# Kernel optimization log

Measured on AMD Instinct MI355X. Metric: run time of the kernel, lower is better.

Reference implementation:

```python
import jax, jax.numpy as jnp
import numpy as np

HEADS = 16
DIM_HEAD = 64
SEG = 512            # total_segment_len (num_longterm_mem_tokens = 0)
THETA = 10000.0
NEG_INF = -1e30


def _rotate_half(t):
    # interleaved pair rotation, as in rotary-embedding-torch
    t2 = t.reshape(*t.shape[:-1], t.shape[-1] // 2, 2)
    return jnp.stack((-t2[..., 1], t2[..., 0]), axis=-1).reshape(t.shape)


def setup_inputs() -> dict:
    key = jax.random.key(0)
    ks = jax.random.split(key, 4)
    b, n, d = 2, 4096, 1024
    dim_inner = HEADS * DIM_HEAD
    seq = jax.random.normal(ks[0], (b, n, d), dtype=jnp.float32)
    g_norm = jnp.ones((d,), dtype=jnp.float32)
    W_qkv = jax.random.normal(ks[1], (d, 3 * dim_inner), dtype=jnp.float32) * (d ** -0.5)
    W_out = jax.random.normal(ks[2], (dim_inner, d), dtype=jnp.float32) * (dim_inner ** -0.5)
    pm = jax.random.normal(ks[3], (2, HEADS, 16, DIM_HEAD), dtype=jnp.float32) * 0.02
    return {"seq": seq, "g_norm": g_norm, "W_qkv": W_qkv, "W_out": W_out, "pm": pm}


def reference(seq, g_norm, W_qkv, W_out, pm):
    b, n_tot, dim = seq.shape
    p = pm.shape[2]
    dh = DIM_HEAD

    # RMSNorm (elementwise affine, eps = dtype eps as in torch default)
    eps = jnp.asarray(jnp.finfo(seq.dtype).eps, seq.dtype)
    x = seq * jax.lax.rsqrt(jnp.mean(seq * seq, axis=-1, keepdims=True) + eps) * g_norm

    qkv = x @ W_qkv                                   # [b, n, 3*h*dh]
    q, k, v = jnp.split(qkv, 3, axis=-1)

    def split_heads(t):
        return t.reshape(b, n_tot, HEADS, dh).transpose(0, 2, 1, 3)  # b h n d

    q, k, v = map(split_heads, (q, k, v))

    # rotary over global positions (applied before segmenting)
    pos = jnp.arange(n_tot, dtype=seq.dtype)
    inv_freq = 1.0 / (THETA ** (jnp.arange(0, dh, 2, dtype=seq.dtype) / dh))
    ang = jnp.repeat(pos[:, None] * inv_freq, 2, axis=-1)            # [n, dh]
    cos, sin = jnp.cos(ang), jnp.sin(ang)
    q = q * cos + _rotate_half(q) * sin
    k = k * cos + _rotate_half(k) * sin

    # fold segments into batch: b h (w n) d -> (b w) h n d
    w = n_tot // SEG
    def seg_fold(t):
        return t.reshape(b, HEADS, w, SEG, dh).transpose(0, 2, 1, 3, 4).reshape(b * w, HEADS, SEG, dh)
    q, k, v = map(seg_fold, (q, k, v))

    # prepend persistent memory kv
    pmk = jnp.broadcast_to(pm[0], (b * w, HEADS, p, dh))
    pmv = jnp.broadcast_to(pm[1], (b * w, HEADS, p, dh))
    k = jnp.concatenate((pmk, k), axis=-2)            # [(bw), h, p+n, d]
    v = jnp.concatenate((pmv, v), axis=-2)

    scores = jnp.einsum('bhid,bhjd->bhij', q, k) * (dh ** -0.5)
    i = jnp.arange(SEG)[:, None]
    j = jnp.arange(SEG + p)[None, :]
    mask = (j < p) | ((j - p) <= i)                   # persistent mem always visible, causal in-segment
    scores = jnp.where(mask, scores, NEG_INF)
    attn = jax.nn.softmax(scores, axis=-1)
    out = jnp.einsum('bhij,bhjd->bhid', attn, v)      # [(bw), h, n, d]

    out = out.transpose(0, 2, 1, 3).reshape(b * w, SEG, HEADS * dh)
    out = out @ W_out
    return out.reshape(b, n_tot, dim)
```

## Files before the change

kernel.cpp:

```cpp
#include <hip/hip_runtime.h>
#include <hip/hip_bf16.h>

typedef __attribute__((ext_vector_type(8))) short short8v;
typedef __attribute__((ext_vector_type(4))) float f32x4;

#define B_ 2
#define NTOK 4096
#define DMODEL 1024
#define HEADS_ 16
#define DH 64
#define SEG_ 512
#define PMEM 16
#define ROWS 8192
#define QKVC 3072

__global__ __launch_bounds__(256) void rmsnorm_bf16(const float* __restrict__ seq,
                                                    const float* __restrict__ g,
                                                    __hip_bfloat16* __restrict__ x) {
    int row = blockIdx.x;
    const float4* in = (const float4*)(seq + (size_t)row * DMODEL);
    int tid = threadIdx.x;
    float4 v = in[tid];
    float ss = v.x*v.x + v.y*v.y + v.z*v.z + v.w*v.w;
    #pragma unroll
    for (int off = 32; off >= 1; off >>= 1) ss += __shfl_xor(ss, off, 64);
    __shared__ float red[4];
    if ((tid & 63) == 0) red[tid >> 6] = ss;
    __syncthreads();
    float tot = red[0] + red[1] + red[2] + red[3];
    float scale = rsqrtf(tot * (1.0f/(float)DMODEL) + 1.1920929e-7f);
    float4 gv = ((const float4*)g)[tid];
    union { ushort4 u; __hip_bfloat16 h[4]; } pk;
    pk.h[0] = __float2bfloat16(v.x*scale*gv.x);
    pk.h[1] = __float2bfloat16(v.y*scale*gv.y);
    pk.h[2] = __float2bfloat16(v.z*scale*gv.z);
    pk.h[3] = __float2bfloat16(v.w*scale*gv.w);
    ((ushort4*)(x + (size_t)row * DMODEL))[tid] = pk.u;
}

__global__ __launch_bounds__(256) void transpose_bf16(const float* __restrict__ W,
                                                      __hip_bfloat16* __restrict__ Wt,
                                                      int K, int N) {
    __shared__ float t[32][33];
    int n0 = blockIdx.x * 32, k0 = blockIdx.y * 32;
    int c = threadIdx.x & 31, r = threadIdx.x >> 5;
    #pragma unroll
    for (int rr = 0; rr < 32; rr += 8)
        t[rr + r][c] = W[(size_t)(k0 + rr + r)*N + n0 + c];
    __syncthreads();
    #pragma unroll
    for (int rr = 0; rr < 32; rr += 8)
        Wt[(size_t)(n0 + rr + r)*K + k0 + c] = __float2bfloat16(t[c][rr + r]);
}

__global__ __launch_bounds__(256) void prep_kernel(float* __restrict__ tab,
                                                   const float* __restrict__ pm,
                                                   __hip_bfloat16* __restrict__ pmb) {
    int idx = blockIdx.x*256 + threadIdx.x;
    if (idx < NTOK*32) {
        int n = idx >> 5, p = idx & 31;
        float inv = powf(10000.f, -(float)p * (1.f/32.f));
        float a = (float)n * inv;
        float sn, cs;
        sincosf(a, &sn, &cs);
        tab[(size_t)n*64 + 2*p]     = cs;
        tab[(size_t)n*64 + 2*p + 1] = sn;
    } else {
        int j = idx - NTOK*32;
        pmb[j] = __float2bfloat16(pm[j]);
    }
}

__device__ __forceinline__ void gldl(const __hip_bfloat16* g, char* l) {
    __builtin_amdgcn_global_load_lds((const __attribute__((address_space(1))) void*)g,
                                     (__attribute__((address_space(3))) void*)l, 16, 0, 0);
}
__device__ __forceinline__ void storeC(float* p, float v) { *p = v; }
__device__ __forceinline__ void storeC(__hip_bfloat16* p, float v) { *p = __float2bfloat16(v); }

template<typename OutT, bool ROPE>
__global__ __launch_bounds__(256, 2) void gemm_t(const __hip_bfloat16* __restrict__ A,
                                                 const __hip_bfloat16* __restrict__ Bt,
                                                 OutT* __restrict__ C,
                                                 const float* __restrict__ tab,
                                                 int M, int N, int K) {
    __shared__ __hip_bfloat16 As[8192];
    __shared__ __hip_bfloat16 Bs[8192];
    const int tid = threadIdx.x;
    const int wid = tid >> 6, lane = tid & 63;
    const int q8 = gridDim.x >> 3;
    const int swz = (blockIdx.x & 7) * q8 + (blockIdx.x >> 3);
    const int nbx = N >> 7;
    const int bm = (swz / nbx) * 128, bn = (swz % nbx) * 128;
    const int wm = (wid >> 1) * 64, wn = (wid & 1) * 64;
    const int fr = lane & 15, g = lane >> 4;

    const __hip_bfloat16* Abase = A  + (size_t)bm * K;
    const __hip_bfloat16* Bbase = Bt + (size_t)bn * K;

    f32x4 acc[4][4];
    #pragma unroll
    for (int i = 0; i < 4; ++i)
        #pragma unroll
        for (int j = 0; j < 4; ++j)
            acc[i][j] = (f32x4){0.f, 0.f, 0.f, 0.f};

    const int srow_in = lane >> 2;
    const int scol8  = (lane & 3) * 8;

    for (int k0 = 0; k0 < K; k0 += 64) {
        #pragma unroll
        for (int m = 0; m < 4; ++m) {
            int p = m & 1, rg = (wid << 1) + (m >> 1);
            gldl(Abase + (size_t)(rg*16 + srow_in)*K + k0 + p*32 + scol8,
                 (char*)(As + p*4096 + rg*512 + lane*8));
        }
        #pragma unroll
        for (int m = 0; m < 4; ++m) {
            int p = m & 1, rg = (wid << 1) + (m >> 1);
            gldl(Bbase + (size_t)(rg*16 + srow_in)*K + k0 + p*32 + scol8,
                 (char*)(Bs + p*4096 + rg*512 + lane*8));
        }
        __syncthreads();

        short8v a[4][2], b[4][2];
        #pragma unroll
        for (int mt = 0; mt < 4; ++mt)
            #pragma unroll
            for (int ks = 0; ks < 2; ++ks)
                a[mt][ks] = *(const short8v*)&As[ks*4096 + (wm + mt*16 + fr)*32 + g*8];
        #pragma unroll
        for (int nt = 0; nt < 4; ++nt)
            #pragma unroll
            for (int ks = 0; ks < 2; ++ks)
                b[nt][ks] = *(const short8v*)&Bs[ks*4096 + (wn + nt*16 + fr)*32 + g*8];
        #pragma unroll
        for (int mt = 0; mt < 4; ++mt)
            #pragma unroll
            for (int nt = 0; nt < 4; ++nt)
                #pragma unroll
                for (int ks = 0; ks < 2; ++ks)
                    acc[mt][nt] = __builtin_amdgcn_mfma_f32_16x16x32_bf16(a[mt][ks], b[nt][ks], acc[mt][nt], 0, 0, 0);
        __syncthreads();
    }

    const int rsub = (lane >> 4) << 2;
    if (ROPE && bn < 2048) {
        #pragma unroll
        for (int mt = 0; mt < 4; ++mt) {
            int rbase = bm + wm + mt*16 + rsub;
            #pragma unroll
            for (int nt = 0; nt < 4; ++nt) {
                int col = bn + wn + nt*16 + fr;
                int d = col & 63;
                int dc = d & ~1;
                #pragma unroll
                for (int r = 0; r < 4; ++r) {
                    float v = acc[mt][nt][r];
                    float pv = __shfl_xor(v, 1, 64);
                    int n = (rbase + r) & (NTOK - 1);
                    const float* tb = tab + (size_t)n*64;
                    float cs = tb[dc], sn = tb[dc+1];
                    float o = v*cs + ((d & 1) ? pv*sn : -pv*sn);
                    storeC(&C[(size_t)(rbase + r)*N + col], (float)o);
                }
            }
        }
    } else {
        #pragma unroll
        for (int mt = 0; mt < 4; ++mt) {
            int rbase = bm + wm + mt*16 + rsub;
            #pragma unroll
            for (int nt = 0; nt < 4; ++nt) {
                int col = bn + wn + nt*16 + fr;
                #pragma unroll
                for (int r = 0; r < 4; ++r)
                    storeC(&C[(size_t)(rbase + r)*N + col], acc[mt][nt][r]);
            }
        }
    }
}

__device__ __forceinline__ void stage_load(const __hip_bfloat16* __restrict__ qkv,
                                           const __hip_bfloat16* __restrict__ pmb,
                                           int h, int srow, int tt, int skey, int sdg,
                                           uint4 kv[2]) {
    int kg = tt*64 + skey;
    if (kg < PMEM) {
        kv[0] = *(const uint4*)(pmb + ((size_t)h*PMEM + kg)*DH + sdg);
        kv[1] = *(const uint4*)(pmb + ((size_t)(HEADS_ + h)*PMEM + kg)*DH + sdg);
    } else {
        int r = min(kg - PMEM, SEG_ - 1);
        const __hip_bfloat16* bp = qkv + (size_t)(srow + r)*QKVC + h*DH + sdg;
        kv[0] = *(const uint4*)(bp + 1024);
        kv[1] = *(const uint4*)(bp + 2048);
    }
}

__device__ __forceinline__ void stage_write(char* Kb, char* Vb,
                                            int skey, int sdg, const uint4 kv[2]) {
    *(uint4*)(Kb + ((skey*128 + sdg*2) ^ ((skey&7)<<4))) = kv[0];
    union { uint4 u; ushort s[8]; } vv; vv.u = kv[1];
    #pragma unroll
    for (int j = 0; j < 8; ++j) {
        int d = sdg + j;
        *(ushort*)(Vb + ((d*128 + skey*2) ^ ((d&7)<<4))) = vv.s[j];
    }
}

__global__ __launch_bounds__(512, 2) void attn_mfma(const __hip_bfloat16* __restrict__ qkv,
                                                    const __hip_bfloat16* __restrict__ pmb,
                                                    __hip_bfloat16* __restrict__ ao) {
    __shared__ __hip_bfloat16 KB[2][4096];
    __shared__ __hip_bfloat16 VB[2][4096];
    __shared__ __hip_bfloat16 PB[8][1024];

    const int s = blockIdx.x, h = blockIdx.y, rb = blockIdx.z;
    const int srow = (s >> 3)*NTOK + (s & 7)*SEG_;
    const int tid = threadIdx.x;
    const int w = tid >> 6, lane = tid & 63;
    const int g = lane >> 4, fr = lane & 15;
    const int rsub = g * 4;
    char* Pw = (char*)&PB[w][0];

    const int grp0 = 2*w + rb;
    const int grp1 = 30 - 2*w + rb;
    const int tmax = 7 + rb;

    short8v aq[2][2];
    #pragma unroll
    for (int mt = 0; mt < 2; ++mt) {
        int grp = mt ? grp1 : grp0;
        const __hip_bfloat16* qp = qkv + (size_t)(srow + grp*16 + fr)*QKVC + h*DH;
        #pragma unroll
        for (int ks = 0; ks < 2; ++ks)
            aq[mt][ks] = *(const short8v*)(qp + ks*32 + g*8);
    }

    f32x4 accO[2][4];
    float m_[2][4], l_[2][4];
    #pragma unroll
    for (int mt = 0; mt < 2; ++mt) {
        #pragma unroll
        for (int dt = 0; dt < 4; ++dt) accO[mt][dt] = (f32x4){0.f,0.f,0.f,0.f};
        #pragma unroll
        for (int r = 0; r < 4; ++r) { m_[mt][r] = -1e30f; l_[mt][r] = 0.f; }
    }

    const int skey = tid >> 3, sdg = (tid & 7) * 8;

    {
        uint4 kv[2];
        stage_load(qkv, pmb, h, srow, 0, skey, sdg, kv);
        stage_write((char*)&KB[0][0], (char*)&VB[0][0], skey, sdg, kv);
    }
    __syncthreads();

    for (int t = 0; t <= tmax; ++t) {
        const int bf = t & 1;
        uint4 kvn[2];
        if (t < tmax) stage_load(qkv, pmb, h, srow, t + 1, skey, sdg, kvn);

        char* Kb = (char*)&KB[bf][0];
        char* Vb = (char*)&VB[bf][0];

        short8v bk[4][2];
        #pragma unroll
        for (int nt = 0; nt < 4; ++nt)
            #pragma unroll
            for (int ks = 0; ks < 2; ++ks) {
                int row = nt*16 + fr;
                bk[nt][ks] = *(const short8v*)(Kb + ((row*128 + ks*64 + g*16) ^ ((row&7)<<4)));
            }

        #pragma unroll
        for (int mt = 0; mt < 2; ++mt) {
            const int qb = (mt ? grp1 : grp0) * 16;
            if (t > 0 && t*64 > qb + 31) continue;

            f32x4 sA[4];
            #pragma unroll
            for (int nt = 0; nt < 4; ++nt) sA[nt] = (f32x4){0.f,0.f,0.f,0.f};
            __builtin_amdgcn_s_setprio(1);
            #pragma unroll
            for (int ks = 0; ks < 2; ++ks)
                #pragma unroll
                for (int nt = 0; nt < 4; ++nt)
                    sA[nt] = __builtin_amdgcn_mfma_f32_16x16x32_bf16(aq[mt][ks], bk[nt][ks], sA[nt], 0, 0, 0);
            __builtin_amdgcn_s_setprio(0);

            if (!(t*64 + 63 <= qb + 16)) {
                #pragma unroll
                for (int nt = 0; nt < 4; ++nt) {
                    int kg2 = t*64 + nt*16 + fr;
                    #pragma unroll
                    for (int r = 0; r < 4; ++r) {
                        int irow = qb + rsub + r;
                        if (!((kg2 < PMEM) || (kg2 <= irow + PMEM))) sA[nt][r] = -1e30f;
                    }
                }
            }

            float mx[4], corr[4];
            #pragma unroll
            for (int r = 0; r < 4; ++r)
                mx[r] = fmaxf(fmaxf(sA[0][r], sA[1][r]), fmaxf(sA[2][r], sA[3][r]));
            #pragma unroll
            for (int r = 0; r < 4; ++r) {
                #pragma unroll
                for (int off = 1; off <= 8; off <<= 1)
                    mx[r] = fmaxf(mx[r], __shfl_xor(mx[r], off, 64));
                float mn = fmaxf(m_[mt][r], mx[r]);
                corr[r] = __expf((m_[mt][r] - mn)*0.125f);
                m_[mt][r] = mn;
            }
            #pragma unroll
            for (int nt = 0; nt < 4; ++nt)
                #pragma unroll
                for (int r = 0; r < 4; ++r)
                    sA[nt][r] = __expf((sA[nt][r] - m_[mt][r])*0.125f);
            #pragma unroll
            for (int r = 0; r < 4; ++r) {
                float lp = sA[0][r] + sA[1][r] + sA[2][r] + sA[3][r];
                l_[mt][r] = l_[mt][r]*corr[r] + lp;
            }
            #pragma unroll
            for (int dt = 0; dt < 4; ++dt)
                #pragma unroll
                for (int r = 0; r < 4; ++r)
                    accO[mt][dt][r] *= corr[r];

            #pragma unroll
            for (int nt = 0; nt < 4; ++nt)
                #pragma unroll
                for (int r = 0; r < 4; ++r) {
                    int row_l = rsub + r;
                    *(__hip_bfloat16*)(Pw + ((row_l*128 + (nt*16 + fr)*2) ^ ((row_l&7)<<4))) =
                        __float2bfloat16(sA[nt][r]);
                }

            __builtin_amdgcn_s_setprio(1);
            #pragma unroll
            for (int ks2 = 0; ks2 < 2; ++ks2) {
                short8v ap = *(const short8v*)(Pw + ((fr*128 + ks2*64 + g*16) ^ ((fr&7)<<4)));
                #pragma unroll
                for (int dt = 0; dt < 4; ++dt) {
                    int vrow = dt*16 + fr;
                    short8v bv = *(const short8v*)(Vb + ((vrow*128 + ks2*64 + g*16) ^ ((vrow&7)<<4)));
                    accO[mt][dt] = __builtin_amdgcn_mfma_f32_16x16x32_bf16(ap, bv, accO[mt][dt], 0, 0, 0);
                }
            }
            __builtin_amdgcn_s_setprio(0);
        }

        if (t < tmax) stage_write((char*)&KB[bf^1][0], (char*)&VB[bf^1][0], skey, sdg, kvn);
        __syncthreads();
    }

    #pragma unroll
    for (int mt = 0; mt < 2; ++mt) {
        const int grp = mt ? grp1 : grp0;
        float inv[4];
        #pragma unroll
        for (int r = 0; r < 4; ++r) {
            float lt = l_[mt][r];
            #pragma unroll
            for (int off = 1; off <= 8; off <<= 1) lt += __shfl_xor(lt, off, 64);
            inv[r] = 1.0f / lt;
        }
        #pragma unroll
        for (int dt = 0; dt < 4; ++dt)
            #pragma unroll
            for (int r = 0; r < 4; ++r) {
                int row_l = rsub + r;
                *(__hip_bfloat16*)(Pw + ((row_l*128 + (dt*16 + fr)*2) ^ ((row_l&7)<<4))) =
                    __float2bfloat16(accO[mt][dt][r] * inv[r]);
            }
        #pragma unroll
        for (int c = 0; c < 2; ++c) {
            int row_l = c*8 + (lane >> 3);
            size_t grow = (size_t)(srow + grp*16 + row_l);
            uint4 v = *(const uint4*)(Pw + ((row_l*128 + (lane&7)*16) ^ ((row_l&7)<<4)));
            *(uint4*)((char*)(ao + grow*DMODEL + h*DH) + (lane&7)*16) = v;
        }
    }
}

extern "C" void kernel_launch(void* const* d_in, const int* in_sizes, int n_in,
                              void* d_out, int out_size, void* d_ws, size_t ws_size,
                              hipStream_t stream) {
    const float* seq  = (const float*)d_in[0];
    const float* g    = (const float*)d_in[1];
    const float* wqkv = (const float*)d_in[2];
    const float* wout = (const float*)d_in[3];
    const float* pm   = (const float*)d_in[4];
    float* out = (float*)d_out;

    char* ws = (char*)d_ws;
    __hip_bfloat16* qkvb  = (__hip_bfloat16*)ws;
    __hip_bfloat16* xb    = (__hip_bfloat16*)(ws + 50331648);
    __hip_bfloat16* wqkvt = (__hip_bfloat16*)(ws + 50331648 + 16777216);
    __hip_bfloat16* woutt = (__hip_bfloat16*)(ws + 50331648 + 16777216 + 6291456);
    float* tab            = (float*)(ws + 50331648 + 16777216 + 6291456 + 2097152);
    __hip_bfloat16* pmb   = (__hip_bfloat16*)(ws + 50331648 + 16777216 + 6291456 + 2097152 + 1048576);

    prep_kernel<<<(NTOK*32 + 2*HEADS_*PMEM*DH)/256, 256, 0, stream>>>(tab, pm, pmb);
    transpose_bf16<<<dim3(QKVC/32, DMODEL/32), 256, 0, stream>>>(wqkv, wqkvt, DMODEL, QKVC);
    transpose_bf16<<<dim3(DMODEL/32, DMODEL/32), 256, 0, stream>>>(wout, woutt, DMODEL, DMODEL);
    rmsnorm_bf16<<<ROWS, 256, 0, stream>>>(seq, g, xb);
    gemm_t<__hip_bfloat16, true><<<(QKVC/128)*(ROWS/128), 256, 0, stream>>>(xb, wqkvt, qkvb, tab, ROWS, QKVC, DMODEL);
    attn_mfma<<<dim3(16, 16, 2), 512, 0, stream>>>(qkvb, pmb, xb);
    gemm_t<float, false><<<(DMODEL/128)*(ROWS/128), 256, 0, stream>>>(xb, woutt, out, nullptr, ROWS, DMODEL, DMODEL);
}
```

Measured before the change: 175.2 us.

## Swizzle GEMM LDS layout and stage QKV epilogue through LDS for vector stores

Merges the A and B shared buffers into one byte array and loads each 128x64 tile as full 128-byte rows with an XOR swizzle on the 16-byte column chunk, so the MFMA fragment reads avoid LDS bank conflicts. For the RoPE/QKV GEMM, the epilogue now writes bf16 results into swizzled shared memory and then copies them out with coalesced 16-byte global stores instead of scattered 2-byte stores. It also reads the cos/sin pair as one float2. The epilogue adds an extra barrier and assumes the output type is bf16 whenever ROPE is set.

```diff
diff --git a/kernel.cpp b/kernel.cpp
--- a/kernel.cpp
+++ b/kernel.cpp
@@ -84,8 +84,7 @@
                                                  OutT* __restrict__ C,
                                                  const float* __restrict__ tab,
                                                  int M, int N, int K) {
-    __shared__ __hip_bfloat16 As[8192];
-    __shared__ __hip_bfloat16 Bs[8192];
+    __shared__ __align__(16) char smem[32768];
     const int tid = threadIdx.x;
     const int wid = tid >> 6, lane = tid & 63;
     const int q8 = gridDim.x >> 3;
@@ -95,8 +94,10 @@
     const int wm = (wid >> 1) * 64, wn = (wid & 1) * 64;
     const int fr = lane & 15, g = lane >> 4;
 
-    const __hip_bfloat16* Abase = A  + (size_t)bm * K;
-    const __hip_bfloat16* Bbase = Bt + (size_t)bn * K;
+    const int srow = tid >> 3;
+    const int scol = ((tid & 7) ^ (srow & 7)) * 8;
+    const __hip_bfloat16* Asrc = A  + (size_t)(bm + srow)*K + scol;
+    const __hip_bfloat16* Bsrc = Bt + (size_t)(bn + srow)*K + scol;
 
     f32x4 acc[4][4];
     #pragma unroll
@@ -105,35 +106,30 @@
         for (int j = 0; j < 4; ++j)
             acc[i][j] = (f32x4){0.f, 0.f, 0.f, 0.f};
 
-    const int srow_in = lane >> 2;
-    const int scol8  = (lane & 3) * 8;
-
     for (int k0 = 0; k0 < K; k0 += 64) {
         #pragma unroll
-        for (int m = 0; m < 4; ++m) {
-            int p = m & 1, rg = (wid << 1) + (m >> 1);
-            gldl(Abase + (size_t)(rg*16 + srow_in)*K + k0 + p*32 + scol8,
-                 (char*)(As + p*4096 + rg*512 + lane*8));
-        }
-        #pragma unroll
-        for (int m = 0; m < 4; ++m) {
-            int p = m & 1, rg = (wid << 1) + (m >> 1);
-            gldl(Bbase + (size_t)(rg*16 + srow_in)*K + k0 + p*32 + scol8,
-                 (char*)(Bs + p*4096 + rg*512 + lane*8));
-        }
+        for (int i = 0; i < 4; ++i)
+            gldl(Asrc + (size_t)i*32*K + k0, smem + i*4096 + tid*16);
+        #pragma unroll
+        for (int i = 0; i < 4; ++i)
+            gldl(Bsrc + (size_t)i*32*K + k0, smem + 16384 + i*4096 + tid*16);
         __syncthreads();
 
         short8v a[4][2], b[4][2];
         #pragma unroll
-        for (int mt = 0; mt < 4; ++mt)
+        for (int mt = 0; mt < 4; ++mt) {
+            int row = wm + mt*16 + fr;
             #pragma unroll
             for (int ks = 0; ks < 2; ++ks)
-                a[mt][ks] = *(const short8v*)&As[ks*4096 + (wm + mt*16 + fr)*32 + g*8];
-        #pragma unroll
-        for (int nt = 0; nt < 4; ++nt)
+                a[mt][ks] = *(const short8v*)(smem + row*128 + ((ks*64 + g*16) ^ ((fr&7)<<4)));
+        }
+        #pragma unroll
+        for (int nt = 0; nt < 4; ++nt) {
+            int row = wn + nt*16 + fr;
             #pragma unroll
             for (int ks = 0; ks < 2; ++ks)
-                b[nt][ks] = *(const short8v*)&Bs[ks*4096 + (wn + nt*16 + fr)*32 + g*8];
+                b[nt][ks] = *(const short8v*)(smem + 16384 + row*128 + ((ks*64 + g*16) ^ ((fr&7)<<4)));
+        }
         #pragma unroll
         for (int mt = 0; mt < 4; ++mt)
             #pragma unroll
@@ -145,26 +141,37 @@
     }
 
     const int rsub = (lane >> 4) << 2;
-    if (ROPE && bn < 2048) {
+    if constexpr (ROPE) {
+        const bool dorope = (bn < 2048);
         #pragma unroll
         for (int mt = 0; mt < 4; ++mt) {
-            int rbase = bm + wm + mt*16 + rsub;
             #pragma unroll
             for (int nt = 0; nt < 4; ++nt) {
-                int col = bn + wn + nt*16 + fr;
-                int d = col & 63;
-                int dc = d & ~1;
+                int colLoc = wn + nt*16 + fr;
+                int d = colLoc & 63, dc = d & ~1;
                 #pragma unroll
                 for (int r = 0; r < 4; ++r) {
+                    int rloc = wm + mt*16 + rsub + r;
                     float v = acc[mt][nt][r];
                     float pv = __shfl_xor(v, 1, 64);
-                    int n = (rbase + r) & (NTOK - 1);
-                    const float* tb = tab + (size_t)n*64;
-                    float cs = tb[dc], sn = tb[dc+1];
-                    float o = v*cs + ((d & 1) ? pv*sn : -pv*sn);
-                    storeC(&C[(size_t)(rbase + r)*N + col], (float)o);
+                    float o = v;
+                    if (dorope) {
+                        int n = (bm + rloc) & (NTOK - 1);
+                        float2 t2 = *(const float2*)&tab[(size_t)n*64 + dc];
+                        o = v*t2.x + ((d & 1) ? pv*t2.y : -pv*t2.y);
+                    }
+                    *(__hip_bfloat16*)(smem + rloc*256 + ((colLoc*2) ^ ((rloc&15)<<4))) =
+                        __float2bfloat16(o);
                 }
             }
+        }
+        __syncthreads();
+        #pragma unroll
+        for (int p = 0; p < 8; ++p) {
+            int idx = p*256 + tid;
+            int rloc = idx >> 4, c16 = idx & 15;
+            uint4 v = *(const uint4*)(smem + rloc*256 + ((c16*16) ^ ((rloc&15)<<4)));
+            *(uint4*)((char*)(C + (size_t)(bm + rloc)*N + bn) + c16*16) = v;
         }
     } else {
         #pragma unroll
```

Result: slower. 188.5 us (+7.6%).
